# Kernel tuning notes

Measured on AMD Instinct MI355X. Metric: run time of the kernel, lower is better.

Reference implementation:

```python
import jax, jax.numpy as jnp
import numpy as np

N_HEADS = 16
D_QK = 64
D_MODEL = 1024
LN_EPS = 1e-6
B, QL, KVL = 2, 2048, 2048


def rms_norm(x, weight, eps=LN_EPS):
    var = jnp.mean(jnp.square(x.astype(jnp.float32)), axis=-1, keepdims=True)
    return (x * jax.lax.rsqrt(var + eps)).astype(x.dtype) * weight


def setup_inputs() -> dict:
    key = jax.random.key(0)
    ks = jax.random.split(key, 5)
    scale_h = 1.0 / np.sqrt(D_MODEL)
    return {
        "q_hidden_states": jax.random.normal(ks[0], (B, QL, D_MODEL), jnp.float32),
        "q_sequence_mask": jnp.ones((B, QL), dtype=bool),
        "kv_hidden_states": jax.random.normal(ks[1], (B, KVL, D_MODEL), jnp.float32),
        "kv_sequence_mask": jnp.ones((B, KVL), dtype=bool),
        "w_q": jax.random.normal(ks[2], (D_MODEL, N_HEADS * D_QK), jnp.float32) * scale_h,
        "w_kv": jax.random.normal(ks[3], (D_MODEL, 2 * N_HEADS * D_QK), jnp.float32) * scale_h,
        "w_o": jax.random.normal(ks[4], (N_HEADS * D_QK, D_MODEL), jnp.float32) * scale_h,
        "ln_weight": jnp.ones((D_MODEL,), jnp.float32),
    }


def reference(q_hidden_states, q_sequence_mask, kv_hidden_states, kv_sequence_mask,
              w_q, w_kv, w_o, ln_weight):
    b, ql, _ = q_hidden_states.shape
    kvl = kv_hidden_states.shape[1]

    normed = rms_norm(q_hidden_states, ln_weight)

    # q projection: [b, ql, H*D] -> [b, H, ql, D]
    q = (normed @ w_q).reshape(b, ql, N_HEADS, D_QK).transpose(0, 2, 1, 3)
    # kv projection: [b, kvl, 2*H*D] -> k, v each [b, H, kvl, D]
    kv = (kv_hidden_states @ w_kv).reshape(b, kvl, 2, N_HEADS, D_QK)
    k = kv[:, :, 0].transpose(0, 2, 1, 3)
    v = kv[:, :, 1].transpose(0, 2, 1, 3)

    # T5 attention: no 1/sqrt(d) scaling
    scores = jnp.einsum("bhqd,bhkd->bhqk", q, k)  # [b, H, ql, kvl]
    attn_mask = q_sequence_mask[:, None, :, None] & kv_sequence_mask[:, None, None, :]
    scores = jnp.where(attn_mask, scores, jnp.finfo(jnp.float32).min)
    attn = jax.nn.softmax(scores.astype(jnp.float32), axis=-1).astype(q.dtype)

    out = jnp.einsum("bhqk,bhkd->bhqd", attn, v)  # [b, H, ql, D]
    out = out.transpose(0, 2, 1, 3).reshape(b, ql, N_HEADS * D_QK)
    out = out @ w_o
    return q_hidden_states + out
```

## Files before the change

### kernel.cpp

```cpp
#include <hip/hip_runtime.h>
#include <stdint.h>

#define BSZ 2
#define QL 2048
#define KVL 2048
#define NH 16
#define DQK 64
#define DM 1024

typedef __bf16 bf16x8 __attribute__((ext_vector_type(8)));
typedef float f32x4 __attribute__((ext_vector_type(4)));

__device__ __forceinline__ ushort f2bf(float f) {
    union { float f; uint32_t u; } c; c.f = f;
    uint32_t u = c.u;
    return (ushort)((u + 0x7fffu + ((u >> 16) & 1u)) >> 16);
}

__device__ __forceinline__ uint32_t pack2bf(float lo, float hi) {
    union { float f; uint32_t u; } a, b;
    a.f = lo; b.f = hi;
    return __builtin_amdgcn_perm(b.u + 0x8000u, a.u + 0x8000u, 0x07060302u);
}

#define GLOAD_LDS16(g, l)                                              \
    __builtin_amdgcn_global_load_lds(                                  \
        (const __attribute__((address_space(1))) uint32_t*)(g),        \
        (__attribute__((address_space(3))) uint32_t*)(l), 16, 0, 0)

__global__ __launch_bounds__(256) void rmsnorm_cast_k(const float* __restrict__ x,
                                                      const float* __restrict__ w,
                                                      ushort* __restrict__ out) {
    int row = blockIdx.x;
    const float4* xr = (const float4*)(x + (size_t)row * DM);
    float4 v = xr[threadIdx.x];
    float s = v.x * v.x + v.y * v.y + v.z * v.z + v.w * v.w;
#pragma unroll
    for (int off = 32; off > 0; off >>= 1) s += __shfl_down(s, off, 64);
    __shared__ float ws4[4];
    if ((threadIdx.x & 63) == 0) ws4[threadIdx.x >> 6] = s;
    __syncthreads();
    float tot = ws4[0] + ws4[1] + ws4[2] + ws4[3];
    float r = rsqrtf(tot * (1.0f / DM) + 1e-6f);
    float4 wv = ((const float4*)w)[threadIdx.x];
    ushort4 o;
    o.x = f2bf(v.x * r * wv.x);
    o.y = f2bf(v.y * r * wv.y);
    o.z = f2bf(v.z * r * wv.z);
    o.w = f2bf(v.w * r * wv.w);
    ((ushort4*)(out + (size_t)row * DM))[threadIdx.x] = o;
}

__global__ __launch_bounds__(256) void prep_k(const float* __restrict__ kv_in,
                                              ushort* __restrict__ kvb,
                                              const float* __restrict__ w_q,
                                              const float* __restrict__ w_kv,
                                              const float* __restrict__ w_o,
                                              ushort* __restrict__ wqT,
                                              ushort* __restrict__ wkvT,
                                              ushort* __restrict__ woT) {
    __shared__ ushort tile[64][65];
    int blk = blockIdx.x;
    int tid = threadIdx.x;
    if (blk < 4096) {
        int i = blk * 256 + tid;
        float4 v = ((const float4*)kv_in)[i];
        ushort4 r;
        r.x = f2bf(v.x); r.y = f2bf(v.y); r.z = f2bf(v.z); r.w = f2bf(v.w);
        ((ushort4*)kvb)[i] = r;
        return;
    }
    int bi = blk - 4096;
    const float* in; ushort* out; int N, bx, by;
    const int K = 1024;
    if (bi < 256)      { in = w_q;  out = wqT;  N = 1024; bx = bi & 15; by = bi >> 4; }
    else if (bi < 768) { int j = bi - 256; in = w_kv; out = wkvT; N = 2048; bx = j & 31; by = j >> 5; }
    else               { int j = bi - 768; in = w_o;  out = woT;  N = 1024; bx = j & 15; by = j >> 4; }
    int k0 = by * 64, n0 = bx * 64;
    int colBase = tid & 63;
    int rowOff = tid >> 6;
#pragma unroll
    for (int i = 0; i < 16; ++i) {
        int row = i * 4 + rowOff;
        tile[colBase][row] = f2bf(in[(size_t)(k0 + row) * N + n0 + colBase]);
    }
    __syncthreads();
#pragma unroll
    for (int i = 0; i < 16; ++i) {
        int nrow = i * 4 + rowOff;
        out[(size_t)(n0 + nrow) * K + k0 + colBase] = tile[nrow][colBase];
    }
}

__global__ __launch_bounds__(256) void transpose_v_k(const ushort* __restrict__ v,
                                                     ushort* __restrict__ vt) {
    int bh = blockIdx.y;
    int t0 = blockIdx.x * 64;
    int lane = threadIdx.x & 63, wave = threadIdx.x >> 6;
    const ushort* src = v + (size_t)bh * KVL * DQK;
    ushort* dst = vt + (size_t)bh * DQK * KVL;
    int t = t0 + lane;
#pragma unroll
    for (int it = 0; it < 2; ++it) {
        int d0 = (wave * 2 + it) * 8;
        union { uint4 u; ushort s[8]; } val;
        val.u = *(const uint4*)&src[(size_t)t * DQK + d0];
#pragma unroll
        for (int j = 0; j < 8; ++j)
            dst[(size_t)(d0 + j) * KVL + t] = val.s[j];
    }
}

__global__ __launch_bounds__(256) void gemm_qkv_k(
    const ushort* __restrict__ normed, const ushort* __restrict__ kvb,
    const ushort* __restrict__ wqT, const ushort* __restrict__ wkvT,
    ushort* __restrict__ q_out, ushort* __restrict__ k_out, ushort* __restrict__ v_out) {
    __shared__ __align__(16) ushort As[128 * 32];
    __shared__ __align__(16) ushort Bs[128 * 32];
    const int K = DM;
    int tid = threadIdx.x;
    int wave = tid >> 6, lane = tid & 63, quad = lane >> 4, l16 = lane & 15;
    int bx = blockIdx.x;
    int isQ = bx < 8;
    const ushort* A = isQ ? normed : kvb;
    const ushort* Bt = isQ ? wqT : wkvT;
    int n0 = (isQ ? bx : bx - 8) * 128;
    int m0 = blockIdx.y * 128;
    int wm = (wave & 1) * 64, wn = (wave >> 1) * 64;

    int r0 = tid >> 2, c0 = (tid & 3) << 3;
    const ushort* ga0 = &A[(size_t)(m0 + r0) * K + c0];
    const ushort* gb0 = &Bt[(size_t)(n0 + r0) * K + c0];

    f32x4 zero = {0.f, 0.f, 0.f, 0.f};
    f32x4 acc[4][4];
#pragma unroll
    for (int i = 0; i < 4; ++i)
#pragma unroll
        for (int j = 0; j < 4; ++j) acc[i][j] = zero;

    for (int k0 = 0; k0 < K; k0 += 32) {
        GLOAD_LDS16(ga0 + k0, &As[tid * 8]);
        GLOAD_LDS16(ga0 + (size_t)64 * K + k0, &As[(tid + 256) * 8]);
        GLOAD_LDS16(gb0 + k0, &Bs[tid * 8]);
        GLOAD_LDS16(gb0 + (size_t)64 * K + k0, &Bs[(tid + 256) * 8]);
        __syncthreads();
        bf16x8 af[4], bfr[4];
#pragma unroll
        for (int mi = 0; mi < 4; ++mi)
            af[mi] = *(const bf16x8*)(&As[(wm + mi * 16 + l16) * 32 + quad * 8]);
#pragma unroll
        for (int ni = 0; ni < 4; ++ni)
            bfr[ni] = *(const bf16x8*)(&Bs[(wn + ni * 16 + l16) * 32 + quad * 8]);
#pragma unroll
        for (int mi = 0; mi < 4; ++mi)
#pragma unroll
            for (int ni = 0; ni < 4; ++ni)
                acc[mi][ni] = __builtin_amdgcn_mfma_f32_16x16x32_bf16(
                    af[mi], bfr[ni], acc[mi][ni], 0, 0, 0);
        __syncthreads();
    }

    const float L2E = 1.44269504089f;
#pragma unroll
    for (int mi = 0; mi < 4; ++mi) {
#pragma unroll
        for (int ni = 0; ni < 4; ++ni) {
#pragma unroll
            for (int r = 0; r < 4; ++r) {
                int mm = m0 + wm + mi * 16 + quad * 4 + r;
                int nn = n0 + wn + ni * 16 + l16;
                float val = acc[mi][ni][r];
                int b = mm >> 11, t = mm & 2047;
                if (isQ) {
                    int h = nn >> 6, d = nn & 63;
                    q_out[((size_t)((b << 4) | h) * QL + t) * DQK + d] = f2bf(val * L2E);
                } else {
                    int c = nn >> 10, h = (nn >> 6) & 15, d = nn & 63;
                    ushort* dst = c ? v_out : k_out;
                    dst[((size_t)((b << 4) | h) * KVL + t) * DQK + d] = f2bf(val);
                }
            }
        }
    }
}

__global__ __launch_bounds__(256) void gemm_o_k(const ushort* __restrict__ A,
                                                const ushort* __restrict__ Bt,
                                                const float* __restrict__ resid,
                                                float* __restrict__ f_out) {
    __shared__ __align__(16) ushort As[64 * 32];
    __shared__ __align__(16) ushort Bs[128 * 32];
    const int K = DM;
    int tid = threadIdx.x;
    int wave = tid >> 6, lane = tid & 63, quad = lane >> 4, l16 = lane & 15;
    int n0 = blockIdx.x * 128, m0 = blockIdx.y * 64;
    int wm = (wave & 1) * 32, wn = (wave >> 1) * 64;

    int r0 = tid >> 2, c0 = (tid & 3) << 3;
    const ushort* ga0 = &A[(size_t)(m0 + r0) * K + c0];
    const ushort* gb0 = &Bt[(size_t)(n0 + r0) * K + c0];

    f32x4 zero = {0.f, 0.f, 0.f, 0.f};
    f32x4 acc[2][4];
#pragma unroll
    for (int i = 0; i < 2; ++i)
#pragma unroll
        for (int j = 0; j < 4; ++j) acc[i][j] = zero;

    for (int k0 = 0; k0 < K; k0 += 32) {
        GLOAD_LDS16(ga0 + k0, &As[tid * 8]);
        GLOAD_LDS16(gb0 + k0, &Bs[tid * 8]);
        GLOAD_LDS16(gb0 + (size_t)64 * K + k0, &Bs[(tid + 256) * 8]);
        __syncthreads();
        bf16x8 af[2], bfr[4];
#pragma unroll
        for (int mi = 0; mi < 2; ++mi)
            af[mi] = *(const bf16x8*)(&As[(wm + mi * 16 + l16) * 32 + quad * 8]);
#pragma unroll
        for (int ni = 0; ni < 4; ++ni)
            bfr[ni] = *(const bf16x8*)(&Bs[(wn + ni * 16 + l16) * 32 + quad * 8]);
#pragma unroll
        for (int mi = 0; mi < 2; ++mi)
#pragma unroll
            for (int ni = 0; ni < 4; ++ni)
                acc[mi][ni] = __builtin_amdgcn_mfma_f32_16x16x32_bf16(
                    af[mi], bfr[ni], acc[mi][ni], 0, 0, 0);
        __syncthreads();
    }

#pragma unroll
    for (int mi = 0; mi < 2; ++mi) {
#pragma unroll
        for (int ni = 0; ni < 4; ++ni) {
#pragma unroll
            for (int r = 0; r < 4; ++r) {
                int mm = m0 + wm + mi * 16 + quad * 4 + r;
                int nn = n0 + wn + ni * 16 + l16;
                size_t o = (size_t)mm * DM + nn;
                f_out[o] = resid[o] + acc[mi][ni][r];
            }
        }
    }
}

__global__ __launch_bounds__(256) void attn_k(const ushort* __restrict__ qh,
                                              const ushort* __restrict__ kh,
                                              const ushort* __restrict__ vt,
                                              ushort* __restrict__ ao) {
    __shared__ __align__(16) ushort smem[2 * 64 * 72 + 8 * 16 * 72];
    ushort* Ks = smem;
    ushort* Vs = smem + 64 * 72;
    ushort* PsB = smem + 2 * 64 * 72;
    int bh = blockIdx.y, bI = bh >> 4, hI = bh & 15;
    int q0 = blockIdx.x * 128;
    int tid = threadIdx.x, wave = tid >> 6, lane = tid & 63;
    int quad = lane >> 4, l16 = lane & 15;
    const ushort* Qp = qh + (size_t)bh * QL * DQK;
    const ushort* Kp = kh + (size_t)bh * KVL * DQK;
    const ushort* Vp = vt + (size_t)bh * DQK * KVL;

    bf16x8 qf[2][2];
#pragma unroll
    for (int g = 0; g < 2; ++g) {
        const ushort* qrow = Qp + (size_t)(q0 + wave * 32 + g * 16 + l16) * DQK;
        qf[g][0] = *(const bf16x8*)(qrow + quad * 8);
        qf[g][1] = *(const bf16x8*)(qrow + 32 + quad * 8);
    }

    int srow = tid >> 3;
    int scol = (tid & 7) << 3;

    f32x4 zero = {0.f, 0.f, 0.f, 0.f};
    f32x4 o[2][4];
#pragma unroll
    for (int g = 0; g < 2; ++g)
#pragma unroll
        for (int i = 0; i < 4; ++i) o[g][i] = zero;
    float lsum[2] = {0.f, 0.f};

    uint4 kr0 = *(const uint4*)&Kp[(size_t)srow * DQK + scol];
    uint4 kr1 = *(const uint4*)&Kp[(size_t)(srow + 32) * DQK + scol];
    uint4 vr0 = *(const uint4*)&Vp[(size_t)srow * KVL + scol];
    uint4 vr1 = *(const uint4*)&Vp[(size_t)(srow + 32) * KVL + scol];

    for (int t0 = 0; t0 < KVL; t0 += 64) {
        *(uint4*)&Ks[srow * 72 + scol] = kr0;
        *(uint4*)&Ks[(srow + 32) * 72 + scol] = kr1;
        *(uint4*)&Vs[srow * 72 + scol] = vr0;
        *(uint4*)&Vs[(srow + 32) * 72 + scol] = vr1;
        __syncthreads();
        int tn = t0 + 64;
        if (tn < KVL) {
            kr0 = *(const uint4*)&Kp[(size_t)(tn + srow) * DQK + scol];
            kr1 = *(const uint4*)&Kp[(size_t)(tn + srow + 32) * DQK + scol];
            vr0 = *(const uint4*)&Vp[(size_t)srow * KVL + tn + scol];
            vr1 = *(const uint4*)&Vp[(size_t)(srow + 32) * KVL + tn + scol];
        }

        f32x4 s[2][4];
#pragma unroll
        for (int mi = 0; mi < 4; ++mi) {
            const ushort* kb = &Ks[(mi * 16 + l16) * 72 + quad * 8];
            bf16x8 kf0 = *(const bf16x8*)kb;
            bf16x8 kf1 = *(const bf16x8*)(kb + 32);
#pragma unroll
            for (int g = 0; g < 2; ++g) {
                f32x4 a = zero;
                a = __builtin_amdgcn_mfma_f32_16x16x32_bf16(kf0, qf[g][0], a, 0, 0, 0);
                a = __builtin_amdgcn_mfma_f32_16x16x32_bf16(kf1, qf[g][1], a, 0, 0, 0);
                s[g][mi] = a;
            }
        }

        bf16x8 pf[2][2];
#pragma unroll
        for (int g = 0; g < 2; ++g) {
            float rs = 0.f;
#pragma unroll
            for (int mi = 0; mi < 4; ++mi)
#pragma unroll
                for (int r = 0; r < 4; ++r) {
                    float p = __builtin_amdgcn_exp2f(s[g][mi][r]);
                    s[g][mi][r] = p;
                    rs += p;
                }
            lsum[g] += rs;
            ushort* prow = &PsB[((wave * 2 + g) * 16 + l16) * 72];
#pragma unroll
            for (int mi = 0; mi < 4; ++mi) {
                uint2 pk;
                pk.x = pack2bf(s[g][mi][0], s[g][mi][1]);
                pk.y = pack2bf(s[g][mi][2], s[g][mi][3]);
                *(uint2*)&prow[mi * 16 + quad * 4] = pk;
            }
            pf[g][0] = *(const bf16x8*)&prow[quad * 8];
            pf[g][1] = *(const bf16x8*)&prow[32 + quad * 8];
        }

#pragma unroll
        for (int mi = 0; mi < 4; ++mi) {
            const ushort* vb = &Vs[(mi * 16 + l16) * 72 + quad * 8];
            bf16x8 vf0 = *(const bf16x8*)vb;
            bf16x8 vf1 = *(const bf16x8*)(vb + 32);
#pragma unroll
            for (int g = 0; g < 2; ++g) {
                o[g][mi] = __builtin_amdgcn_mfma_f32_16x16x32_bf16(vf0, pf[g][0], o[g][mi], 0, 0, 0);
                o[g][mi] = __builtin_amdgcn_mfma_f32_16x16x32_bf16(vf1, pf[g][1], o[g][mi], 0, 0, 0);
            }
        }
        __syncthreads();
    }

#pragma unroll
    for (int g = 0; g < 2; ++g) {
        float lg = lsum[g];
        lg += __shfl_xor(lg, 16, 64);
        lg += __shfl_xor(lg, 32, 64);
        float rinv = __builtin_amdgcn_rcpf(lg);
        ushort* orow = &smem[(size_t)(wave * 32 + g * 16 + l16) * 72];
#pragma unroll
        for (int mi = 0; mi < 4; ++mi) {
            uint2 pk;
            pk.x = pack2bf(o[g][mi][0] * rinv, o[g][mi][1] * rinv);
            pk.y = pack2bf(o[g][mi][2] * rinv, o[g][mi][3] * rinv);
            *(uint2*)&orow[mi * 16 + quad * 4] = pk;
        }
    }
    __syncthreads();
#pragma unroll
    for (int it = 0; it < 4; ++it) {
        int idx = tid + it * 256;
        int ql = idx >> 3, c = (idx & 7) << 3;
        uint4 vv = *(const uint4*)&smem[ql * 72 + c];
        *(uint4*)&ao[((size_t)(bI * QL + q0 + ql)) * DM + hI * 64 + c] = vv;
    }
}

extern "C" void kernel_launch(void* const* d_in, const int* in_sizes, int n_in,
                              void* d_out, int out_size, void* d_ws, size_t ws_size,
                              hipStream_t stream) {
    (void)in_sizes; (void)n_in; (void)out_size; (void)ws_size;
    const float* qh_in = (const float*)d_in[0];
    const float* kv_in = (const float*)d_in[2];
    const float* w_q  = (const float*)d_in[4];
    const float* w_kv = (const float*)d_in[5];
    const float* w_o  = (const float*)d_in[6];
    const float* lnw  = (const float*)d_in[7];
    float* out = (float*)d_out;

    char* ws = (char*)d_ws;
    ushort* normed = (ushort*)(ws);
    ushort* vT     = (ushort*)(ws);
    ushort* kvb    = (ushort*)(ws + ((size_t)8 << 20));
    ushort* wqT    = (ushort*)(ws + ((size_t)16 << 20));
    ushort* wkvT   = (ushort*)(ws + ((size_t)18 << 20));
    ushort* woT    = (ushort*)(ws + ((size_t)22 << 20));
    ushort* qheads = (ushort*)(ws + ((size_t)24 << 20));
    ushort* kheads = (ushort*)(ws + ((size_t)32 << 20));
    ushort* vheads = (ushort*)(ws + ((size_t)40 << 20));
    ushort* attno  = (ushort*)(ws + ((size_t)48 << 20));

    rmsnorm_cast_k<<<BSZ * QL, 256, 0, stream>>>(qh_in, lnw, normed);
    prep_k<<<4096 + 1024, 256, 0, stream>>>(kv_in, kvb, w_q, w_kv, w_o, wqT, wkvT, woT);

    gemm_qkv_k<<<dim3(24, 32), 256, 0, stream>>>(normed, kvb, wqT, wkvT,
                                                 qheads, kheads, vheads);
    transpose_v_k<<<dim3(KVL / 64, BSZ * NH), 256, 0, stream>>>(vheads, vT);
    attn_k<<<dim3(QL / 128, BSZ * NH), 256, 0, stream>>>(qheads, kheads, vT, attno);
    gemm_o_k<<<dim3(8, 64), 256, 0, stream>>>(attno, woT, qh_in, out);
}
```

Baseline: 218.8 us.

## Split attention over KV halves, fuse V transpose and RMSNorm into producers

Attention now runs as a two-way split over the KV sequence, doubling the grid. Each half writes unnormalised partial outputs and row sums, and a new combine kernel merges them and normalises. The V transpose is folded into the QKV GEMM epilogue, which writes V directly in transposed layout. RMSNorm is merged into the prep kernel, removing two launches and one intermediate pass over V. In exchange it adds an extra partial-output round trip through memory and a bf16 rounding of the partials, and it relies on the softmax using no per-half running max.

```diff
diff --git a/kernel.cpp b/kernel.cpp
--- a/kernel.cpp
+++ b/kernel.cpp
@@ -23,35 +23,22 @@
     return __builtin_amdgcn_perm(b.u + 0x8000u, a.u + 0x8000u, 0x07060302u);
 }
 
+__device__ __forceinline__ float bflo(uint32_t w) {
+    union { uint32_t u; float f; } c; c.u = w << 16; return c.f;
+}
+__device__ __forceinline__ float bfhi(uint32_t w) {
+    union { uint32_t u; float f; } c; c.u = w & 0xffff0000u; return c.f;
+}
+
 #define GLOAD_LDS16(g, l)                                              \
     __builtin_amdgcn_global_load_lds(                                  \
         (const __attribute__((address_space(1))) uint32_t*)(g),        \
         (__attribute__((address_space(3))) uint32_t*)(l), 16, 0, 0)
 
-__global__ __launch_bounds__(256) void rmsnorm_cast_k(const float* __restrict__ x,
-                                                      const float* __restrict__ w,
-                                                      ushort* __restrict__ out) {
-    int row = blockIdx.x;
-    const float4* xr = (const float4*)(x + (size_t)row * DM);
-    float4 v = xr[threadIdx.x];
-    float s = v.x * v.x + v.y * v.y + v.z * v.z + v.w * v.w;
-#pragma unroll
-    for (int off = 32; off > 0; off >>= 1) s += __shfl_down(s, off, 64);
-    __shared__ float ws4[4];
-    if ((threadIdx.x & 63) == 0) ws4[threadIdx.x >> 6] = s;
-    __syncthreads();
-    float tot = ws4[0] + ws4[1] + ws4[2] + ws4[3];
-    float r = rsqrtf(tot * (1.0f / DM) + 1e-6f);
-    float4 wv = ((const float4*)w)[threadIdx.x];
-    ushort4 o;
-    o.x = f2bf(v.x * r * wv.x);
-    o.y = f2bf(v.y * r * wv.y);
-    o.z = f2bf(v.z * r * wv.z);
-    o.w = f2bf(v.w * r * wv.w);
-    ((ushort4*)(out + (size_t)row * DM))[threadIdx.x] = o;
-}
-
-__global__ __launch_bounds__(256) void prep_k(const float* __restrict__ kv_in,
+__global__ __launch_bounds__(256) void prep_k(const float* __restrict__ qh_in,
+                                              const float* __restrict__ lnw,
+                                              ushort* __restrict__ normed,
+                                              const float* __restrict__ kv_in,
                                               ushort* __restrict__ kvb,
                                               const float* __restrict__ w_q,
                                               const float* __restrict__ w_kv,
@@ -59,18 +46,39 @@
                                               ushort* __restrict__ wqT,
                                               ushort* __restrict__ wkvT,
                                               ushort* __restrict__ woT) {
-    __shared__ ushort tile[64][65];
     int blk = blockIdx.x;
     int tid = threadIdx.x;
     if (blk < 4096) {
-        int i = blk * 256 + tid;
+        int row = blk;
+        const float4* xr = (const float4*)(qh_in + (size_t)row * DM);
+        float4 v = xr[tid];
+        float s = v.x * v.x + v.y * v.y + v.z * v.z + v.w * v.w;
+#pragma unroll
+        for (int off = 32; off > 0; off >>= 1) s += __shfl_down(s, off, 64);
+        __shared__ float ws4[4];
+        if ((tid & 63) == 0) ws4[tid >> 6] = s;
+        __syncthreads();
+        float tot = ws4[0] + ws4[1] + ws4[2] + ws4[3];
+        float r = rsqrtf(tot * (1.0f / DM) + 1e-6f);
+        float4 wv = ((const float4*)lnw)[tid];
+        ushort4 o;
+        o.x = f2bf(v.x * r * wv.x);
+        o.y = f2bf(v.y * r * wv.y);
+        o.z = f2bf(v.z * r * wv.z);
+        o.w = f2bf(v.w * r * wv.w);
+        ((ushort4*)(normed + (size_t)row * DM))[tid] = o;
+        return;
+    }
+    if (blk < 8192) {
+        int i = (blk - 4096) * 256 + tid;
         float4 v = ((const float4*)kv_in)[i];
         ushort4 r;
         r.x = f2bf(v.x); r.y = f2bf(v.y); r.z = f2bf(v.z); r.w = f2bf(v.w);
         ((ushort4*)kvb)[i] = r;
         return;
     }
-    int bi = blk - 4096;
+    __shared__ ushort tile[64][65];
+    int bi = blk - 8192;
     const float* in; ushort* out; int N, bx, by;
     const int K = 1024;
     if (bi < 256)      { in = w_q;  out = wqT;  N = 1024; bx = bi & 15; by = bi >> 4; }
@@ -92,29 +100,10 @@
     }
 }
 
-__global__ __launch_bounds__(256) void transpose_v_k(const ushort* __restrict__ v,
-                                                     ushort* __restrict__ vt) {
-    int bh = blockIdx.y;
-    int t0 = blockIdx.x * 64;
-    int lane = threadIdx.x & 63, wave = threadIdx.x >> 6;
-    const ushort* src = v + (size_t)bh * KVL * DQK;
-    ushort* dst = vt + (size_t)bh * DQK * KVL;
-    int t = t0 + lane;
-#pragma unroll
-    for (int it = 0; it < 2; ++it) {
-        int d0 = (wave * 2 + it) * 8;
-        union { uint4 u; ushort s[8]; } val;
-        val.u = *(const uint4*)&src[(size_t)t * DQK + d0];
-#pragma unroll
-        for (int j = 0; j < 8; ++j)
-            dst[(size_t)(d0 + j) * KVL + t] = val.s[j];
-    }
-}
-
 __global__ __launch_bounds__(256) void gemm_qkv_k(
     const ushort* __restrict__ normed, const ushort* __restrict__ kvb,
     const ushort* __restrict__ wqT, const ushort* __restrict__ wkvT,
-    ushort* __restrict__ q_out, ushort* __restrict__ k_out, ushort* __restrict__ v_out) {
+    ushort* __restrict__ q_out, ushort* __restrict__ k_out, ushort* __restrict__ vt_out) {
     __shared__ __align__(16) ushort As[128 * 32];
     __shared__ __align__(16) ushort Bs[128 * 32];
     const int K = DM;
@@ -162,24 +151,49 @@
     }
 
     const float L2E = 1.44269504089f;
-#pragma unroll
-    for (int mi = 0; mi < 4; ++mi) {
-#pragma unroll
-        for (int ni = 0; ni < 4; ++ni) {
-#pragma unroll
-            for (int r = 0; r < 4; ++r) {
-                int mm = m0 + wm + mi * 16 + quad * 4 + r;
-                int nn = n0 + wn + ni * 16 + l16;
-                float val = acc[mi][ni][r];
-                int b = mm >> 11, t = mm & 2047;
-                if (isQ) {
-                    int h = nn >> 6, d = nn & 63;
-                    q_out[((size_t)((b << 4) | h) * QL + t) * DQK + d] = f2bf(val * L2E);
-                } else {
-                    int c = nn >> 10, h = (nn >> 6) & 15, d = nn & 63;
-                    ushort* dst = c ? v_out : k_out;
-                    dst[((size_t)((b << 4) | h) * KVL + t) * DQK + d] = f2bf(val);
-                }
+    if (isQ) {
+        int h = (n0 + wn) >> 6;
+#pragma unroll
+        for (int mi = 0; mi < 4; ++mi) {
+            int mm = m0 + wm + mi * 16 + quad * 4;
+            int b = mm >> 11, t = mm & 2047;
+            ushort* dst = &q_out[((size_t)((b << 4) | h) * QL + t) * DQK];
+#pragma unroll
+            for (int ni = 0; ni < 4; ++ni) {
+                int d = ni * 16 + l16;
+#pragma unroll
+                for (int r = 0; r < 4; ++r)
+                    dst[(size_t)r * DQK + d] = f2bf(acc[mi][ni][r] * L2E);
+            }
+        }
+    } else if (((n0 + wn) >> 10) == 0) {
+        int h = (n0 + wn) >> 6;
+#pragma unroll
+        for (int mi = 0; mi < 4; ++mi) {
+            int mm = m0 + wm + mi * 16 + quad * 4;
+            int b = mm >> 11, t = mm & 2047;
+            ushort* dst = &k_out[((size_t)((b << 4) | h) * QL + t) * DQK];
+#pragma unroll
+            for (int ni = 0; ni < 4; ++ni) {
+                int d = ni * 16 + l16;
+#pragma unroll
+                for (int r = 0; r < 4; ++r)
+                    dst[(size_t)r * DQK + d] = f2bf(acc[mi][ni][r]);
+            }
+        }
+    } else {
+        int h = ((n0 + wn) >> 6) & 15;
+#pragma unroll
+        for (int mi = 0; mi < 4; ++mi) {
+            int mm = m0 + wm + mi * 16 + quad * 4;
+            int b = mm >> 11, t = mm & 2047;
+#pragma unroll
+            for (int ni = 0; ni < 4; ++ni) {
+                int d = ni * 16 + l16;
+                uint2 pk;
+                pk.x = pack2bf(acc[mi][ni][0], acc[mi][ni][1]);
+                pk.y = pack2bf(acc[mi][ni][2], acc[mi][ni][3]);
+                *(uint2*)&vt_out[((size_t)(((b << 4) | h) * DQK + d)) * KVL + t] = pk;
             }
         }
     }
@@ -247,13 +261,16 @@
 __global__ __launch_bounds__(256) void attn_k(const ushort* __restrict__ qh,
                                               const ushort* __restrict__ kh,
                                               const ushort* __restrict__ vt,
-                                              ushort* __restrict__ ao) {
+                                              ushort* __restrict__ o_part,
+                                              float* __restrict__ l_part) {
     __shared__ __align__(16) ushort smem[2 * 64 * 72 + 8 * 16 * 72];
     ushort* Ks = smem;
     ushort* Vs = smem + 64 * 72;
     ushort* PsB = smem + 2 * 64 * 72;
-    int bh = blockIdx.y, bI = bh >> 4, hI = bh & 15;
+    int bh = blockIdx.y;
     int q0 = blockIdx.x * 128;
+    int half = blockIdx.z;
+    int tbase = half * (KVL / 2);
     int tid = threadIdx.x, wave = tid >> 6, lane = tid & 63;
     int quad = lane >> 4, l16 = lane & 15;
     const ushort* Qp = qh + (size_t)bh * QL * DQK;
@@ -279,19 +296,19 @@
         for (int i = 0; i < 4; ++i) o[g][i] = zero;
     float lsum[2] = {0.f, 0.f};
 
-    uint4 kr0 = *(const uint4*)&Kp[(size_t)srow * DQK + scol];
-    uint4 kr1 = *(const uint4*)&Kp[(size_t)(srow + 32) * DQK + scol];
-    uint4 vr0 = *(const uint4*)&Vp[(size_t)srow * KVL + scol];
-    uint4 vr1 = *(const uint4*)&Vp[(size_t)(srow + 32) * KVL + scol];
-
-    for (int t0 = 0; t0 < KVL; t0 += 64) {
+    uint4 kr0 = *(const uint4*)&Kp[(size_t)(tbase + srow) * DQK + scol];
+    uint4 kr1 = *(const uint4*)&Kp[(size_t)(tbase + srow + 32) * DQK + scol];
+    uint4 vr0 = *(const uint4*)&Vp[(size_t)srow * KVL + tbase + scol];
+    uint4 vr1 = *(const uint4*)&Vp[(size_t)(srow + 32) * KVL + tbase + scol];
+
+    for (int t0 = tbase; t0 < tbase + KVL / 2; t0 += 64) {
         *(uint4*)&Ks[srow * 72 + scol] = kr0;
         *(uint4*)&Ks[(srow + 32) * 72 + scol] = kr1;
         *(uint4*)&Vs[srow * 72 + scol] = vr0;
         *(uint4*)&Vs[(srow + 32) * 72 + scol] = vr1;
         __syncthreads();
         int tn = t0 + 64;
-        if (tn < KVL) {
+        if (tn < tbase + KVL / 2) {
             kr0 = *(const uint4*)&Kp[(size_t)(tn + srow) * DQK + scol];
             kr1 = *(const uint4*)&Kp[(size_t)(tn + srow + 32) * DQK + scol];
             vr0 = *(const uint4*)&Vp[(size_t)srow * KVL + tn + scol];
@@ -357,24 +374,40 @@
         float lg = lsum[g];
         lg += __shfl_xor(lg, 16, 64);
         lg += __shfl_xor(lg, 32, 64);
-        float rinv = __builtin_amdgcn_rcpf(lg);
-        ushort* orow = &smem[(size_t)(wave * 32 + g * 16 + l16) * 72];
+        int q = q0 + wave * 32 + g * 16 + l16;
+        size_t base = (size_t)(half * 32 + bh) * QL + q;
+        if (quad == 0) l_part[base] = lg;
+        ushort* ob = &o_part[base * DQK];
 #pragma unroll
         for (int mi = 0; mi < 4; ++mi) {
             uint2 pk;
-            pk.x = pack2bf(o[g][mi][0] * rinv, o[g][mi][1] * rinv);
-            pk.y = pack2bf(o[g][mi][2] * rinv, o[g][mi][3] * rinv);
-            *(uint2*)&orow[mi * 16 + quad * 4] = pk;
-        }
-    }
-    __syncthreads();
-#pragma unroll
-    for (int it = 0; it < 4; ++it) {
-        int idx = tid + it * 256;
-        int ql = idx >> 3, c = (idx & 7) << 3;
-        uint4 vv = *(const uint4*)&smem[ql * 72 + c];
-        *(uint4*)&ao[((size_t)(bI * QL + q0 + ql)) * DM + hI * 64 + c] = vv;
-    }
+            pk.x = pack2bf(o[g][mi][0], o[g][mi][1]);
+            pk.y = pack2bf(o[g][mi][2], o[g][mi][3]);
+            *(uint2*)&ob[mi * 16 + quad * 4] = pk;
+        }
+    }
+}
+
+__global__ __launch_bounds__(256) void combine_k(const ushort* __restrict__ o_part,
+                                                 const float* __restrict__ l_part,
+                                                 ushort* __restrict__ attno) {
+    int flat = blockIdx.x * 256 + threadIdx.x;
+    int bh = flat >> 14;
+    int rem = flat & 16383;
+    int q = rem >> 3;
+    int dc = rem & 7;
+    size_t base = (size_t)bh * QL + q;
+    const size_t halfStride = (size_t)32 * QL;
+    float l = l_part[base] + l_part[base + halfStride];
+    float rinv = __builtin_amdgcn_rcpf(l);
+    const uint4 a = *(const uint4*)&o_part[base * DQK + dc * 8];
+    const uint4 b = *(const uint4*)&o_part[(base + halfStride) * DQK + dc * 8];
+    uint4 res;
+    res.x = pack2bf((bflo(a.x) + bflo(b.x)) * rinv, (bfhi(a.x) + bfhi(b.x)) * rinv);
+    res.y = pack2bf((bflo(a.y) + bflo(b.y)) * rinv, (bfhi(a.y) + bfhi(b.y)) * rinv);
+    res.z = pack2bf((bflo(a.z) + bflo(b.z)) * rinv, (bfhi(a.z) + bfhi(b.z)) * rinv);
+    res.w = pack2bf((bflo(a.w) + bflo(b.w)) * rinv, (bfhi(a.w) + bfhi(b.w)) * rinv);
+    *(uint4*)&attno[((size_t)((bh >> 4) * QL + q)) * DM + (bh & 15) * 64 + dc * 8] = res;
 }
 
 extern "C" void kernel_launch(void* const* d_in, const int* in_sizes, int n_in,
@@ -391,22 +424,23 @@
 
     char* ws = (char*)d_ws;
     ushort* normed = (ushort*)(ws);
-    ushort* vT     = (ushort*)(ws);
     ushort* kvb    = (ushort*)(ws + ((size_t)8 << 20));
+    ushort* o_part = (ushort*)(ws);
     ushort* wqT    = (ushort*)(ws + ((size_t)16 << 20));
+    float*  l_part = (float*)(ws + ((size_t)16 << 20));
     ushort* wkvT   = (ushort*)(ws + ((size_t)18 << 20));
     ushort* woT    = (ushort*)(ws + ((size_t)22 << 20));
     ushort* qheads = (ushort*)(ws + ((size_t)24 << 20));
     ushort* kheads = (ushort*)(ws + ((size_t)32 << 20));
-    ushort* vheads = (ushort*)(ws + ((size_t)40 << 20));
+    ushort* vT     = (ushort*)(ws + ((size_t)40 << 20));
     ushort* attno  = (ushort*)(ws + ((size_t)48 << 20));
 
-    rmsnorm_cast_k<<<BSZ * QL, 256, 0, stream>>>(qh_in, lnw, normed);
-    prep_k<<<4096 + 1024, 256, 0, stream>>>(kv_in, kvb, w_q, w_kv, w_o, wqT, wkvT, woT);
-
+    prep_k<<<9216, 256, 0, stream>>>(qh_in, lnw, normed, kv_in, kvb,
+                                     w_q, w_kv, w_o, wqT, wkvT, woT);
     gemm_qkv_k<<<dim3(24, 32), 256, 0, stream>>>(normed, kvb, wqT, wkvT,
-                                                 qheads, kheads, vheads);
-    transpose_v_k<<<dim3(KVL / 64, BSZ * NH), 256, 0, stream>>>(vheads, vT);
-    attn_k<<<dim3(QL / 128, BSZ * NH), 256, 0, stream>>>(qheads, kheads, vT, attno);
+                                                 qheads, kheads, vT);
+    attn_k<<<dim3(QL / 128, BSZ * NH, 2), 256, 0, stream>>>(qheads, kheads, vT,
+                                                            o_part, l_part);
+    combine_k<<<2048, 256, 0, stream>>>(o_part, l_part, attno);
     gemm_o_k<<<dim3(8, 64), 256, 0, stream>>>(attno, woT, qh_in, out);
 }
```

Measured after the change: 226.5 us. +3.5%, slower.

## Fuse rmsnorm into prep, write V transposed from QKV GEMM, MFMA row sums

Applied to the files above, without the earlier changes.

Merges the rmsnorm kernel into the prep kernel and removes the separate V transpose kernel. The QKV GEMM epilogue now stages its output tile through LDS and writes Q/K with 16-byte stores and V directly in transposed layout. In attention, the softmax row sums are computed with an extra MFMA against a ones vector instead of scalar adds, and probabilities are packed to bf16 by truncation instead of rounding. This cuts two launches, an extra pass over V, and scattered 2-byte stores, at the cost of more LDS use in the GEMM and slightly less precise probabilities and row sums.

```diff
diff --git a/kernel.cpp b/kernel.cpp
--- a/kernel.cpp
+++ b/kernel.cpp
@@ -23,35 +23,21 @@
     return __builtin_amdgcn_perm(b.u + 0x8000u, a.u + 0x8000u, 0x07060302u);
 }
 
+__device__ __forceinline__ uint32_t pack2bf_t(float lo, float hi) {
+    union { float f; uint32_t u; } a, b;
+    a.f = lo; b.f = hi;
+    return __builtin_amdgcn_perm(b.u, a.u, 0x07060302u);
+}
+
 #define GLOAD_LDS16(g, l)                                              \
     __builtin_amdgcn_global_load_lds(                                  \
         (const __attribute__((address_space(1))) uint32_t*)(g),        \
         (__attribute__((address_space(3))) uint32_t*)(l), 16, 0, 0)
 
-__global__ __launch_bounds__(256) void rmsnorm_cast_k(const float* __restrict__ x,
-                                                      const float* __restrict__ w,
-                                                      ushort* __restrict__ out) {
-    int row = blockIdx.x;
-    const float4* xr = (const float4*)(x + (size_t)row * DM);
-    float4 v = xr[threadIdx.x];
-    float s = v.x * v.x + v.y * v.y + v.z * v.z + v.w * v.w;
-#pragma unroll
-    for (int off = 32; off > 0; off >>= 1) s += __shfl_down(s, off, 64);
-    __shared__ float ws4[4];
-    if ((threadIdx.x & 63) == 0) ws4[threadIdx.x >> 6] = s;
-    __syncthreads();
-    float tot = ws4[0] + ws4[1] + ws4[2] + ws4[3];
-    float r = rsqrtf(tot * (1.0f / DM) + 1e-6f);
-    float4 wv = ((const float4*)w)[threadIdx.x];
-    ushort4 o;
-    o.x = f2bf(v.x * r * wv.x);
-    o.y = f2bf(v.y * r * wv.y);
-    o.z = f2bf(v.z * r * wv.z);
-    o.w = f2bf(v.w * r * wv.w);
-    ((ushort4*)(out + (size_t)row * DM))[threadIdx.x] = o;
-}
-
-__global__ __launch_bounds__(256) void prep_k(const float* __restrict__ kv_in,
+__global__ __launch_bounds__(256) void prep_k(const float* __restrict__ qh_in,
+                                              const float* __restrict__ lnw,
+                                              ushort* __restrict__ normed,
+                                              const float* __restrict__ kv_in,
                                               ushort* __restrict__ kvb,
                                               const float* __restrict__ w_q,
                                               const float* __restrict__ w_kv,
@@ -59,18 +45,39 @@
                                               ushort* __restrict__ wqT,
                                               ushort* __restrict__ wkvT,
                                               ushort* __restrict__ woT) {
-    __shared__ ushort tile[64][65];
     int blk = blockIdx.x;
     int tid = threadIdx.x;
     if (blk < 4096) {
-        int i = blk * 256 + tid;
+        int row = blk;
+        const float4* xr = (const float4*)(qh_in + (size_t)row * DM);
+        float4 v = xr[tid];
+        float s = v.x * v.x + v.y * v.y + v.z * v.z + v.w * v.w;
+#pragma unroll
+        for (int off = 32; off > 0; off >>= 1) s += __shfl_down(s, off, 64);
+        __shared__ float ws4[4];
+        if ((tid & 63) == 0) ws4[tid >> 6] = s;
+        __syncthreads();
+        float tot = ws4[0] + ws4[1] + ws4[2] + ws4[3];
+        float r = rsqrtf(tot * (1.0f / DM) + 1e-6f);
+        float4 wv = ((const float4*)lnw)[tid];
+        ushort4 o;
+        o.x = f2bf(v.x * r * wv.x);
+        o.y = f2bf(v.y * r * wv.y);
+        o.z = f2bf(v.z * r * wv.z);
+        o.w = f2bf(v.w * r * wv.w);
+        ((ushort4*)(normed + (size_t)row * DM))[tid] = o;
+        return;
+    }
+    if (blk < 8192) {
+        int i = (blk - 4096) * 256 + tid;
         float4 v = ((const float4*)kv_in)[i];
         ushort4 r;
         r.x = f2bf(v.x); r.y = f2bf(v.y); r.z = f2bf(v.z); r.w = f2bf(v.w);
         ((ushort4*)kvb)[i] = r;
         return;
     }
-    int bi = blk - 4096;
+    __shared__ ushort tile[64][65];
+    int bi = blk - 8192;
     const float* in; ushort* out; int N, bx, by;
     const int K = 1024;
     if (bi < 256)      { in = w_q;  out = wqT;  N = 1024; bx = bi & 15; by = bi >> 4; }
@@ -92,31 +99,13 @@
     }
 }
 
-__global__ __launch_bounds__(256) void transpose_v_k(const ushort* __restrict__ v,
-                                                     ushort* __restrict__ vt) {
-    int bh = blockIdx.y;
-    int t0 = blockIdx.x * 64;
-    int lane = threadIdx.x & 63, wave = threadIdx.x >> 6;
-    const ushort* src = v + (size_t)bh * KVL * DQK;
-    ushort* dst = vt + (size_t)bh * DQK * KVL;
-    int t = t0 + lane;
-#pragma unroll
-    for (int it = 0; it < 2; ++it) {
-        int d0 = (wave * 2 + it) * 8;
-        union { uint4 u; ushort s[8]; } val;
-        val.u = *(const uint4*)&src[(size_t)t * DQK + d0];
-#pragma unroll
-        for (int j = 0; j < 8; ++j)
-            dst[(size_t)(d0 + j) * KVL + t] = val.s[j];
-    }
-}
-
 __global__ __launch_bounds__(256) void gemm_qkv_k(
     const ushort* __restrict__ normed, const ushort* __restrict__ kvb,
     const ushort* __restrict__ wqT, const ushort* __restrict__ wkvT,
-    ushort* __restrict__ q_out, ushort* __restrict__ k_out, ushort* __restrict__ v_out) {
-    __shared__ __align__(16) ushort As[128 * 32];
-    __shared__ __align__(16) ushort Bs[128 * 32];
+    ushort* __restrict__ q_out, ushort* __restrict__ k_out, ushort* __restrict__ vt_out) {
+    __shared__ __align__(16) ushort smem[16896];
+    ushort* As = smem;
+    ushort* Bs = smem + 4096;
     const int K = DM;
     int tid = threadIdx.x;
     int wave = tid >> 6, lane = tid & 63, quad = lane >> 4, l16 = lane & 15;
@@ -162,25 +151,56 @@
     }
 
     const float L2E = 1.44269504089f;
-#pragma unroll
-    for (int mi = 0; mi < 4; ++mi) {
-#pragma unroll
-        for (int ni = 0; ni < 4; ++ni) {
-#pragma unroll
-            for (int r = 0; r < 4; ++r) {
-                int mm = m0 + wm + mi * 16 + quad * 4 + r;
-                int nn = n0 + wn + ni * 16 + l16;
-                float val = acc[mi][ni][r];
-                int b = mm >> 11, t = mm & 2047;
-                if (isQ) {
-                    int h = nn >> 6, d = nn & 63;
-                    q_out[((size_t)((b << 4) | h) * QL + t) * DQK + d] = f2bf(val * L2E);
-                } else {
-                    int c = nn >> 10, h = (nn >> 6) & 15, d = nn & 63;
-                    ushort* dst = c ? v_out : k_out;
-                    dst[((size_t)((b << 4) | h) * KVL + t) * DQK + d] = f2bf(val);
+    int b = m0 >> 11, m0t = m0 & 2047;
+    if (bx < 16) {
+        float sc = isQ ? L2E : 1.0f;
+        ushort* dst0 = isQ ? q_out : k_out;
+#pragma unroll
+        for (int mi = 0; mi < 4; ++mi) {
+            int t_loc = wm + mi * 16 + quad * 4;
+#pragma unroll
+            for (int ni = 0; ni < 4; ++ni) {
+                int n_loc = wn + ni * 16 + l16;
+#pragma unroll
+                for (int r = 0; r < 4; ++r) {
+                    union { float f; uint32_t u; } c;
+                    c.f = acc[mi][ni][r] * sc;
+                    smem[(t_loc + r) * 132 + n_loc] = (ushort)((c.u + 0x8000u) >> 16);
                 }
             }
+        }
+        __syncthreads();
+        int hb = (n0 >> 6) & 15;
+#pragma unroll
+        for (int it = 0; it < 8; ++it) {
+            int idx = it * 256 + tid;
+            int t = idx >> 4, ch = (idx & 15) << 3;
+            int h = hb + (ch >> 6), d = ch & 63;
+            uint4 vv = *(const uint4*)&smem[t * 132 + ch];
+            *(uint4*)&dst0[((size_t)((b << 4) | h) * QL + m0t + t) * DQK + d] = vv;
+        }
+    } else {
+        int hbase = (n0 >> 6) & 15;
+        int rbase = ((b << 4) | hbase) * 64;
+#pragma unroll
+        for (int mi = 0; mi < 4; ++mi) {
+            int t_loc = wm + mi * 16 + quad * 4;
+#pragma unroll
+            for (int ni = 0; ni < 4; ++ni) {
+                int n_loc = wn + ni * 16 + l16;
+                uint2 pk;
+                pk.x = pack2bf(acc[mi][ni][0], acc[mi][ni][1]);
+                pk.y = pack2bf(acc[mi][ni][2], acc[mi][ni][3]);
+                *(uint2*)&smem[n_loc * 132 + t_loc] = pk;
+            }
+        }
+        __syncthreads();
+#pragma unroll
+        for (int it = 0; it < 8; ++it) {
+            int idx = it * 256 + tid;
+            int n = idx >> 4, ch = (idx & 15) << 3;
+            uint4 vv = *(const uint4*)&smem[n * 132 + ch];
+            *(uint4*)&vt_out[((size_t)(rbase + n)) * KVL + m0t + ch] = vv;
         }
     }
 }
@@ -268,16 +288,22 @@
         qf[g][1] = *(const bf16x8*)(qrow + 32 + quad * 8);
     }
 
+    bf16x8 onef;
+#pragma unroll
+    for (int j = 0; j < 8; ++j) onef[j] = (l16 == 0) ? (__bf16)1.0f : (__bf16)0.0f;
+
     int srow = tid >> 3;
     int scol = (tid & 7) << 3;
 
     f32x4 zero = {0.f, 0.f, 0.f, 0.f};
     f32x4 o[2][4];
-#pragma unroll
-    for (int g = 0; g < 2; ++g)
+    f32x4 lacc[2];
+#pragma unroll
+    for (int g = 0; g < 2; ++g) {
+        lacc[g] = zero;
 #pragma unroll
         for (int i = 0; i < 4; ++i) o[g][i] = zero;
-    float lsum[2] = {0.f, 0.f};
+    }
 
     uint4 kr0 = *(const uint4*)&Kp[(size_t)srow * DQK + scol];
     uint4 kr1 = *(const uint4*)&Kp[(size_t)(srow + 32) * DQK + scol];
@@ -316,26 +342,23 @@
         bf16x8 pf[2][2];
 #pragma unroll
         for (int g = 0; g < 2; ++g) {
-            float rs = 0.f;
 #pragma unroll
             for (int mi = 0; mi < 4; ++mi)
 #pragma unroll
-                for (int r = 0; r < 4; ++r) {
-                    float p = __builtin_amdgcn_exp2f(s[g][mi][r]);
-                    s[g][mi][r] = p;
-                    rs += p;
-                }
-            lsum[g] += rs;
+                for (int r = 0; r < 4; ++r)
+                    s[g][mi][r] = __builtin_amdgcn_exp2f(s[g][mi][r]);
             ushort* prow = &PsB[((wave * 2 + g) * 16 + l16) * 72];
 #pragma unroll
             for (int mi = 0; mi < 4; ++mi) {
                 uint2 pk;
-                pk.x = pack2bf(s[g][mi][0], s[g][mi][1]);
-                pk.y = pack2bf(s[g][mi][2], s[g][mi][3]);
+                pk.x = pack2bf_t(s[g][mi][0], s[g][mi][1]);
+                pk.y = pack2bf_t(s[g][mi][2], s[g][mi][3]);
                 *(uint2*)&prow[mi * 16 + quad * 4] = pk;
             }
             pf[g][0] = *(const bf16x8*)&prow[quad * 8];
             pf[g][1] = *(const bf16x8*)&prow[32 + quad * 8];
+            lacc[g] = __builtin_amdgcn_mfma_f32_16x16x32_bf16(onef, pf[g][0], lacc[g], 0, 0, 0);
+            lacc[g] = __builtin_amdgcn_mfma_f32_16x16x32_bf16(onef, pf[g][1], lacc[g], 0, 0, 0);
         }
 
 #pragma unroll
@@ -354,7 +377,7 @@
 
 #pragma unroll
     for (int g = 0; g < 2; ++g) {
-        float lg = lsum[g];
+        float lg = lacc[g][0];
         lg += __shfl_xor(lg, 16, 64);
         lg += __shfl_xor(lg, 32, 64);
         float rinv = __builtin_amdgcn_rcpf(lg);
@@ -391,22 +414,19 @@
 
     char* ws = (char*)d_ws;
     ushort* normed = (ushort*)(ws);
-    ushort* vT     = (ushort*)(ws);
     ushort* kvb    = (ushort*)(ws + ((size_t)8 << 20));
     ushort* wqT    = (ushort*)(ws + ((size_t)16 << 20));
     ushort* wkvT   = (ushort*)(ws + ((size_t)18 << 20));
     ushort* woT    = (ushort*)(ws + ((size_t)22 << 20));
     ushort* qheads = (ushort*)(ws + ((size_t)24 << 20));
     ushort* kheads = (ushort*)(ws + ((size_t)32 << 20));
-    ushort* vheads = (ushort*)(ws + ((size_t)40 << 20));
+    ushort* vT     = (ushort*)(ws + ((size_t)40 << 20));
     ushort* attno  = (ushort*)(ws + ((size_t)48 << 20));
 
-    rmsnorm_cast_k<<<BSZ * QL, 256, 0, stream>>>(qh_in, lnw, normed);
-    prep_k<<<4096 + 1024, 256, 0, stream>>>(kv_in, kvb, w_q, w_kv, w_o, wqT, wkvT, woT);
-
+    prep_k<<<9216, 256, 0, stream>>>(qh_in, lnw, normed, kv_in, kvb,
+                                     w_q, w_kv, w_o, wqT, wkvT, woT);
     gemm_qkv_k<<<dim3(24, 32), 256, 0, stream>>>(normed, kvb, wqT, wkvT,
-                                                 qheads, kheads, vheads);
-    transpose_v_k<<<dim3(KVL / 64, BSZ * NH), 256, 0, stream>>>(vheads, vT);
+                                                 qheads, kheads, vT);
     attn_k<<<dim3(QL / 128, BSZ * NH), 256, 0, stream>>>(qheads, kheads, vT, attno);
     gemm_o_k<<<dim3(8, 64), 256, 0, stream>>>(attno, woT, qh_in, out);
 }
```

Result: no change. 220.7 us (+0.9%).
